# Performance work log

Measured on AMD Instinct MI355X. Metric: run time of the kernel, lower is better.

Reference implementation:

```python
import jax, jax.numpy as jnp
import numpy as np

N, E, D, H, C, B, G = 50000, 800000, 128, 256, 40, 3, 2
EPS = 1e-5


def setup_inputs() -> dict:
    key = jax.random.key(0)
    ks = jax.random.split(key, 32)
    rn = lambda k, s: jax.random.normal(k, s, dtype=jnp.float32)
    inp = {
        'x': rn(ks[0], (N, D)),
        'edge_index': jax.random.randint(ks[1], (2, E), 0, N, dtype=jnp.int64),
        'Wp': rn(ks[2], (D, H)), 'bp': rn(ks[3], (H,)),
        'W1l': rn(ks[4], (B, H, H)), 'b1l': rn(ks[5], (B, H)), 'W1r': rn(ks[6], (B, H, H)),
        'W2l': rn(ks[7], (B, H, H)), 'b2l': rn(ks[8], (B, H)), 'W2r': rn(ks[9], (B, H, H)),
        'bn1_g': rn(ks[10], (B, H)), 'bn1_b': rn(ks[11], (B, H)), 'bn1_m': rn(ks[12], (B, H)),
        'bn1_v': jax.random.uniform(ks[13], (B, H), dtype=jnp.float32),
        'bn2_g': rn(ks[14], (B, H)), 'bn2_b': rn(ks[15], (B, H)), 'bn2_m': rn(ks[16], (B, H)),
        'bn2_v': jax.random.uniform(ks[17], (B, H), dtype=jnp.float32),
        'gate_W': rn(ks[18], (G, H, H)), 'gate_b': rn(ks[19], (G, H)),
        'Wc1': rn(ks[20], (H, H // 2)), 'bc1': rn(ks[21], (H // 2,)),
        'Wc2': rn(ks[22], (H // 2, C)), 'bc2': rn(ks[23], (C,)),
    }
    return inp


def _sage(x, src, dst, Wl, bl, Wr):
    # PyG SAGEConv (mean aggr): lin_l(mean_{j in N(i)} x_j) + lin_r(x_i)
    agg = jax.ops.segment_sum(x[src], dst, num_segments=N)  # [N,H]
    cnt = jax.ops.segment_sum(jnp.ones((src.shape[0],), x.dtype), dst, num_segments=N)
    mean = agg / jnp.maximum(cnt, 1.0)[:, None]
    return mean @ Wl + bl + x @ Wr


def _bn(x, g, b, m, v):
    return (x - m) * (g * jax.lax.rsqrt(v + EPS)) + b


def reference(x, edge_index, Wp, bp, W1l, b1l, W1r, W2l, b2l, W2r,
              bn1_g, bn1_b, bn1_m, bn1_v, bn2_g, bn2_b, bn2_m, bn2_v,
              gate_W, gate_b, Wc1, bc1, Wc2, bc2):
    src, dst = edge_index[0], edge_index[1]
    prev = x @ Wp + bp  # input projection [N,H]
    for i in range(B):
        res = prev
        h = jax.nn.relu(_bn(_sage(prev, src, dst, W1l[i], b1l[i], W1r[i]),
                            bn1_g[i], bn1_b[i], bn1_m[i], bn1_v[i]))
        h = jax.nn.relu(_bn(_sage(h, src, dst, W2l[i], b2l[i], W2r[i]),
                            bn2_g[i], bn2_b[i], bn2_m[i], bn2_v[i]))
        cur = h + res
        if i > 0:
            gate = jax.nn.sigmoid(prev @ gate_W[i - 1] + gate_b[i - 1])
            cur = gate * prev + (1.0 - gate) * cur
        prev = cur
    return jax.nn.relu(prev @ Wc1 + bc1) @ Wc2 + bc2  # [N,C]
```

## Files before the change

kernel.cpp:

```cpp
#include <hip/hip_runtime.h>
#include <hip/hip_bf16.h>
#include <cstdint>

#define NNODES 50000
#define MPAD   50048
#define NEDGES 800000
#define DIN 128
#define HID 256
#define NCLS 40
#define NBLK 3
#define EPSV 1e-5f

typedef __bf16 bf16x8 __attribute__((ext_vector_type(8)));
typedef float  f32x4  __attribute__((ext_vector_type(4)));
typedef unsigned short us4v __attribute__((ext_vector_type(4)));
typedef unsigned short us8v __attribute__((ext_vector_type(8)));

__device__ __forceinline__ unsigned short bf_rtn(float x) {
  unsigned u = __float_as_uint(x);
  return (unsigned short)((u + 0x7fffu + ((u >> 16) & 1u)) >> 16);
}
__device__ __forceinline__ float bf_f(unsigned short h) {
  return __uint_as_float((unsigned)h << 16);
}
__device__ __forceinline__ void split4(float4 a, us4v& h, us4v& m, us4v& l) {
  float v[4] = {a.x, a.y, a.z, a.w};
#pragma unroll
  for (int i = 0; i < 4; i++) {
    unsigned short hh = bf_rtn(v[i]);
    float r1 = v[i] - bf_f(hh);
    unsigned short mm = bf_rtn(r1);
    float r2 = r1 - bf_f(mm);
    h[i] = hh; m[i] = mm; l[i] = bf_rtn(r2);
  }
}

__device__ __forceinline__ void glds16(const void* gsrc, void* ldst) {
  __builtin_amdgcn_global_load_lds((const __attribute__((address_space(1))) void*)gsrc,
                                   (__attribute__((address_space(3))) void*)ldst,
                                   16, 0, 0);
}

__global__ void hist_kernel(const int* __restrict__ dst, int* __restrict__ cnt, int E) {
  int e = blockIdx.x * blockDim.x + threadIdx.x;
  if (e < E) atomicAdd(&cnt[dst[e]], 1);
}

__global__ void scan_kernel(const int* __restrict__ cnt, int* __restrict__ row_ptr,
                            float* __restrict__ inv_cnt, int N) {
  __shared__ int sums[1024];
  int t = threadIdx.x;
  int chunk = (N + 1023) >> 10;
  int beg = t * chunk;
  int end = beg + chunk; if (end > N) end = N;
  int s = 0;
  for (int i = beg; i < end; ++i) s += cnt[i];
  sums[t] = s;
  __syncthreads();
  for (int off = 1; off < 1024; off <<= 1) {
    int v = 0;
    if (t >= off) v = sums[t - off];
    __syncthreads();
    sums[t] += v;
    __syncthreads();
  }
  int run = (t == 0) ? 0 : sums[t - 1];
  for (int i = beg; i < end; ++i) {
    row_ptr[i] = run;
    int c = cnt[i];
    inv_cnt[i] = 1.0f / (float)(c > 0 ? c : 1);
    run += c;
  }
  if (t == 1023) row_ptr[N] = run;
}

__global__ void fill_kernel(const int* __restrict__ src, const int* __restrict__ dst,
                            const int* __restrict__ row_ptr, int* __restrict__ fillc,
                            int* __restrict__ col, int E) {
  int e = blockIdx.x * blockDim.x + threadIdx.x;
  if (e < E) {
    int d = dst[e];
    int pos = atomicAdd(&fillc[d], 1);
    col[row_ptr[d] + pos] = src[e];
  }
}

__global__ __launch_bounds__(256)
void agg_kernel(const float* __restrict__ x, float* __restrict__ out,
                const int* __restrict__ row_ptr, const int* __restrict__ col,
                const float* __restrict__ inv_cnt) {
  int n = blockIdx.x;
  int h = threadIdx.x;
  int beg = row_ptr[n], end = row_ptr[n + 1];
  float s = 0.0f;
  for (int j = beg; j < end; ++j) {
    int c = col[j];
    s += x[(long)c * HID + h];
  }
  out[(long)n * HID + h] = s * inv_cnt[n];
}

__global__ void fold_kernel(const float* __restrict__ b1l, const float* __restrict__ g1,
                            const float* __restrict__ bb1, const float* __restrict__ m1,
                            const float* __restrict__ v1,
                            const float* __restrict__ b2l, const float* __restrict__ g2,
                            const float* __restrict__ bb2, const float* __restrict__ m2,
                            const float* __restrict__ v2,
                            float* __restrict__ S1, float* __restrict__ T1,
                            float* __restrict__ S2, float* __restrict__ T2) {
  int idx = blockIdx.x * 256 + threadIdx.x;
  float s1 = g1[idx] * rsqrtf(v1[idx] + EPSV);
  S1[idx] = s1;
  T1[idx] = (b1l[idx] - m1[idx]) * s1 + bb1[idx];
  float s2 = g2[idx] * rsqrtf(v2[idx] + EPSV);
  S2[idx] = s2;
  T2[idx] = (b2l[idx] - m2[idx]) * s2 + bb2[idx];
}

#define PREP_TOTAL 368640
struct PrepDescs {
  const float* src[16];
  unsigned dst_off[16];
  int N[16];
  int cum[16];
};
__global__ __launch_bounds__(256)
void prep_kernel(PrepDescs pd, char* out) {
  int i = blockIdx.x * 256 + threadIdx.x;
  if (i >= PREP_TOTAL) return;
  int j = 0;
  while (i >= pd.cum[j]) j++;
  int li = i - (j ? pd.cum[j - 1] : 0);
  int c = li % 12;
  int t = li / 12;
  int N = pd.N[j];
  int n = t % N;
  int kt = t / N;
  const float* src = pd.src[j];
  char* base = out + pd.dst_off[j] + (size_t)kt * N * 192;
  int p, k8;
  size_t addr;
  if (c < 8) {
    int d = c ^ (n & 7);
    p = d >> 2; k8 = d & 3;
    addr = (size_t)n * 128 + (size_t)c * 16;
  } else {
    p = 2; k8 = c - 8;
    addr = (size_t)N * 128 + ((size_t)k8 * N + n) * 16;
  }
  us8v v;
#pragma unroll
  for (int xj = 0; xj < 8; xj++) {
    float w = src[(size_t)(kt * 32 + k8 * 8 + xj) * N + n];
    unsigned short h = bf_rtn(w);
    if (p == 0) { v[xj] = h; continue; }
    float r1 = w - bf_f(h);
    unsigned short m = bf_rtn(r1);
    v[xj] = (p == 1) ? m : bf_rtn(r1 - bf_f(m));
  }
  *reinterpret_cast<us8v*>(base + addr) = v;
}

template<int BN, bool GATED>
__global__ __launch_bounds__(256)
void gemm_mfma(const float* __restrict__ A1, const char* __restrict__ B1, int K1,
               const float* __restrict__ A2, const char* __restrict__ B2, int K2,
               const char* __restrict__ BG, const float* __restrict__ Gb,
               const float* __restrict__ Sc, const float* __restrict__ Tc,
               const float* __restrict__ resid, float* __restrict__ C,
               int Mguard, int do_relu) {
  constexpr int NT = BN / 64;
  constexpr int NG = (BN * 48) / 1024;
  __shared__ __align__(16) unsigned short A_lds[64][104];
  __shared__ __align__(16) char B_lds[BN * 192];
  const int tid  = threadIdx.x;
  const int wv   = tid >> 6;
  const int lane = tid & 63;
  const int l15  = lane & 15;
  const int quad = lane >> 4;
  const int m0   = blockIdx.x * 64;
  const int sm  = tid >> 3;
  const int skc = (tid & 7) * 4;

  f32x4 acc1[4][NT];
#pragma unroll
  for (int i = 0; i < 4; i++)
#pragma unroll
    for (int j = 0; j < NT; j++) acc1[i][j] = (f32x4){0.f, 0.f, 0.f, 0.f};
  f32x4 acc2[GATED ? 4 : 1][GATED ? NT : 1];
  if constexpr (GATED) {
#pragma unroll
    for (int i = 0; i < 4; i++)
#pragma unroll
      for (int j = 0; j < NT; j++) acc2[i][j] = (f32x4){0.f, 0.f, 0.f, 0.f};
  }

  auto phase = [&](const float* __restrict__ A, const char* __restrict__ Bp,
                   int K, f32x4 (&acc)[4][NT]) {
    const int KT = K / 32;
    const bool g0 = (m0 + sm) < Mguard;
    const bool g1 = (m0 + 32 + sm) < Mguard;
    const float* ap0 = A + (size_t)(m0 + sm) * K + skc;
    const float* ap1 = A + (size_t)(m0 + 32 + sm) * K + skc;
    for (int kt = 0; kt < KT; ++kt) {
      __syncthreads();
      const char* bsrc = Bp + (size_t)kt * (BN * 192) + wv * (BN * 48) + (size_t)lane * 16;
      char* bdst = B_lds + wv * (BN * 48);
#pragma unroll
      for (int j = 0; j < NG; ++j)
        glds16(bsrc + j * 1024, bdst + j * 1024);
      float4 a0 = make_float4(0.f, 0.f, 0.f, 0.f), a1 = a0;
      if (g0) a0 = *reinterpret_cast<const float4*>(ap0 + kt * 32);
      if (g1) a1 = *reinterpret_cast<const float4*>(ap1 + kt * 32);
      us4v h4, m4, l4;
      split4(a0, h4, m4, l4);
      *reinterpret_cast<us4v*>(&A_lds[sm][skc])      = h4;
      *reinterpret_cast<us4v*>(&A_lds[sm][32 + skc]) = m4;
      *reinterpret_cast<us4v*>(&A_lds[sm][64 + skc]) = l4;
      split4(a1, h4, m4, l4);
      *reinterpret_cast<us4v*>(&A_lds[32 + sm][skc])      = h4;
      *reinterpret_cast<us4v*>(&A_lds[32 + sm][32 + skc]) = m4;
      *reinterpret_cast<us4v*>(&A_lds[32 + sm][64 + skc]) = l4;
      __syncthreads();
      bf16x8 ah[4], am[4], al[4];
#pragma unroll
      for (int mt = 0; mt < 4; mt++) {
        const unsigned short* rp = &A_lds[mt * 16 + l15][0];
        ah[mt] = *reinterpret_cast<const bf16x8*>(rp + quad * 8);
        am[mt] = *reinterpret_cast<const bf16x8*>(rp + 32 + quad * 8);
        al[mt] = *reinterpret_cast<const bf16x8*>(rp + 64 + quad * 8);
      }
#pragma unroll
      for (int nt = 0; nt < NT; nt++) {
        int n = wv * (BN / 4) + nt * 16 + l15;
        int sw = n & 7;
        const char* rb = B_lds + (size_t)n * 128;
        bf16x8 bh = *reinterpret_cast<const bf16x8*>(rb + ((quad ^ sw) * 16));
        bf16x8 bm = *reinterpret_cast<const bf16x8*>(rb + (((4 + quad) ^ sw) * 16));
        bf16x8 bl = *reinterpret_cast<const bf16x8*>(
            B_lds + (size_t)BN * 128 + ((size_t)quad * BN + n) * 16);
#pragma unroll
        for (int mt = 0; mt < 4; mt++) {
          acc[mt][nt] = __builtin_amdgcn_mfma_f32_16x16x32_bf16(ah[mt], bh, acc[mt][nt], 0, 0, 0);
          acc[mt][nt] = __builtin_amdgcn_mfma_f32_16x16x32_bf16(ah[mt], bm, acc[mt][nt], 0, 0, 0);
          acc[mt][nt] = __builtin_amdgcn_mfma_f32_16x16x32_bf16(am[mt], bh, acc[mt][nt], 0, 0, 0);
          acc[mt][nt] = __builtin_amdgcn_mfma_f32_16x16x32_bf16(am[mt], bm, acc[mt][nt], 0, 0, 0);
          acc[mt][nt] = __builtin_amdgcn_mfma_f32_16x16x32_bf16(ah[mt], bl, acc[mt][nt], 0, 0, 0);
          acc[mt][nt] = __builtin_amdgcn_mfma_f32_16x16x32_bf16(al[mt], bh, acc[mt][nt], 0, 0, 0);
        }
      }
    }
  };

  phase(A1, B1, K1, acc1);
  if (A2) phase(A2, B2, K2, acc1);
  if constexpr (GATED) phase(resid, BG, HID, acc2);

#pragma unroll
  for (int nt = 0; nt < NT; nt++) {
    int colc = wv * (BN / 4) + nt * 16 + l15;
    float sc = Sc ? Sc[colc] : 1.0f;
    float tc = Tc[colc];
    float gb = 0.0f;
    if constexpr (GATED) gb = Gb[colc];
#pragma unroll
    for (int mt = 0; mt < 4; mt++) {
#pragma unroll
      for (int r = 0; r < 4; r++) {
        int row = m0 + mt * 16 + quad * 4 + r;
        size_t base = (size_t)row * BN + colc;
        float v = acc1[mt][nt][r] * sc + tc;
        if (do_relu) v = fmaxf(v, 0.0f);
        if constexpr (GATED) {
          float p = resid[base];
          float g = 1.0f / (1.0f + __expf(-(acc2[mt][nt][r] + gb)));
          v = g * p + (1.0f - g) * (v + p);
        } else if (resid) {
          v += resid[base];
        }
        C[base] = v;
      }
    }
  }
}

__global__ __launch_bounds__(256)
void classifier2(const float* __restrict__ Tin, const float* __restrict__ W,
                 const float* __restrict__ bias, float* __restrict__ out, int M) {
  __shared__ float Ws[DIN * NCLS];
  __shared__ float bs[NCLS];
  __shared__ float Ts[64][DIN + 4];
  int tid = threadIdx.x;
  for (int i = tid; i < DIN * NCLS; i += 256) Ws[i] = W[i];
  if (tid < NCLS) bs[tid] = bias[tid];
  int row0 = blockIdx.x * 64;
  for (int idx = tid; idx < 64 * (DIN / 4); idx += 256) {
    int r = idx / (DIN / 4);
    int c4 = idx % (DIN / 4);
    float4 v = make_float4(0.f, 0.f, 0.f, 0.f);
    if (row0 + r < M) v = *reinterpret_cast<const float4*>(Tin + (long)(row0 + r) * DIN + c4 * 4);
    *reinterpret_cast<float4*>(&Ts[r][c4 * 4]) = v;
  }
  __syncthreads();
  int r = tid >> 2;
  int c0 = (tid & 3) * 10;
  float s[10];
#pragma unroll
  for (int c = 0; c < 10; c++) s[c] = bs[c0 + c];
  for (int k = 0; k < DIN; k++) {
    float a = Ts[r][k];
#pragma unroll
    for (int c = 0; c < 10; c++) s[c] = fmaf(a, Ws[k * NCLS + c0 + c], s[c]);
  }
  if (row0 + r < M) {
#pragma unroll
    for (int c = 0; c < 10; c++) out[(long)(row0 + r) * NCLS + c0 + c] = s[c];
  }
}

extern "C" void kernel_launch(void* const* d_in, const int* in_sizes, int n_in,
                              void* d_out, int out_size, void* d_ws, size_t ws_size,
                              hipStream_t stream) {
  const float* x      = (const float*)d_in[0];
  const int*   ei     = (const int*)d_in[1];
  const float* Wp     = (const float*)d_in[2];
  const float* bp     = (const float*)d_in[3];
  const float* W1l    = (const float*)d_in[4];
  const float* b1l    = (const float*)d_in[5];
  const float* W1r    = (const float*)d_in[6];
  const float* W2l    = (const float*)d_in[7];
  const float* b2l    = (const float*)d_in[8];
  const float* W2r    = (const float*)d_in[9];
  const float* bn1_g  = (const float*)d_in[10];
  const float* bn1_b  = (const float*)d_in[11];
  const float* bn1_m  = (const float*)d_in[12];
  const float* bn1_v  = (const float*)d_in[13];
  const float* bn2_g  = (const float*)d_in[14];
  const float* bn2_b  = (const float*)d_in[15];
  const float* bn2_m  = (const float*)d_in[16];
  const float* bn2_v  = (const float*)d_in[17];
  const float* gate_W = (const float*)d_in[18];
  const float* gate_b = (const float*)d_in[19];
  const float* Wc1    = (const float*)d_in[20];
  const float* bc1    = (const float*)d_in[21];
  const float* Wc2    = (const float*)d_in[22];
  const float* bc2    = (const float*)d_in[23];
  const int* srcp = ei;
  const int* dstp = ei + NEDGES;

  char* wsb = (char*)d_ws;
  size_t off = 0;
  auto alloc = [&](size_t bytes) -> void* {
    void* p = wsb + off;
    off += (bytes + 255) & ~(size_t)255;
    return p;
  };
  float* X0 = (float*)alloc((size_t)MPAD * HID * 4);
  float* X1 = (float*)alloc((size_t)MPAD * HID * 4);
  float* X2 = (float*)alloc((size_t)MPAD * HID * 4);
  char* prep = (char*)alloc(5898240);
  int* cnt     = (int*)alloc((size_t)NNODES * 4 * 2);
  int* fillc   = cnt + NNODES;
  int* row_ptr = (int*)alloc((size_t)(NNODES + 1) * 4);
  float* inv   = (float*)alloc((size_t)NNODES * 4);
  int* col     = (int*)alloc((size_t)NEDGES * 4);
  float* S1 = (float*)alloc(NBLK * HID * 4);
  float* T1 = (float*)alloc(NBLK * HID * 4);
  float* S2 = (float*)alloc(NBLK * HID * 4);
  float* T2 = (float*)alloc(NBLK * HID * 4);

  auto poff = [](int idx) -> unsigned {
    if (idx == 0) return 0;
    return 196608u + (unsigned)(idx - 1) * 393216u;
  };
  const char* prepWp  = prep + poff(0);
  auto prepW1l = [&](int i) { return prep + poff(1 + i); };
  auto prepW1r = [&](int i) { return prep + poff(4 + i); };
  auto prepW2l = [&](int i) { return prep + poff(7 + i); };
  auto prepW2r = [&](int i) { return prep + poff(10 + i); };
  auto prepGate = [&](int g) { return prep + poff(13 + g); };
  const char* prepWc1 = prep + poff(15);

  PrepDescs pd;
  {
    int c = 0, k = 0;
    auto add = [&](const float* s, int N, int chunks, unsigned doff) {
      pd.src[k] = s; pd.N[k] = N; c += chunks; pd.cum[k] = c; pd.dst_off[k] = doff; k++;
    };
    add(Wp, 256, 12288, poff(0));
    for (int i = 0; i < 3; i++) add(W1l + (size_t)i * 65536, 256, 24576, poff(1 + i));
    for (int i = 0; i < 3; i++) add(W1r + (size_t)i * 65536, 256, 24576, poff(4 + i));
    for (int i = 0; i < 3; i++) add(W2l + (size_t)i * 65536, 256, 24576, poff(7 + i));
    for (int i = 0; i < 3; i++) add(W2r + (size_t)i * 65536, 256, 24576, poff(10 + i));
    for (int g = 0; g < 2; g++) add(gate_W + (size_t)g * 65536, 256, 24576, poff(13 + g));
    add(Wc1, 128, 12288, poff(15));
  }

  hipMemsetAsync(cnt, 0, (size_t)NNODES * 4 * 2, stream);
  int eb = (NEDGES + 255) / 256;
  hist_kernel<<<eb, 256, 0, stream>>>(dstp, cnt, NEDGES);
  scan_kernel<<<1, 1024, 0, stream>>>(cnt, row_ptr, inv, NNODES);
  fill_kernel<<<eb, 256, 0, stream>>>(srcp, dstp, row_ptr, fillc, col, NEDGES);
  fold_kernel<<<3, 256, 0, stream>>>(b1l, bn1_g, bn1_b, bn1_m, bn1_v,
                                     b2l, bn2_g, bn2_b, bn2_m, bn2_v, S1, T1, S2, T2);
  prep_kernel<<<PREP_TOTAL / 256, 256, 0, stream>>>(pd, prep);

  int gm = MPAD / 64;
  gemm_mfma<256, false><<<gm, 256, 0, stream>>>(
      x, prepWp, DIN, nullptr, nullptr, 0, nullptr, nullptr,
      nullptr, bp, nullptr, X0, NNODES, 0);

  float* bufs[3] = {X0, X1, X2};
  int prev = 0;
  for (int i = 0; i < NBLK; ++i) {
    int bm = (prev + 1) % 3;
    int bh = (prev + 2) % 3;
    float* P  = bufs[prev];
    float* Mb = bufs[bm];
    float* Hb = bufs[bh];
    agg_kernel<<<NNODES, 256, 0, stream>>>(P, Mb, row_ptr, col, inv);
    gemm_mfma<256, false><<<gm, 256, 0, stream>>>(
        Mb, prepW1l(i), HID, P, prepW1r(i), HID, nullptr, nullptr,
        S1 + i * HID, T1 + i * HID, nullptr, Hb, MPAD, 1);
    agg_kernel<<<NNODES, 256, 0, stream>>>(Hb, Mb, row_ptr, col, inv);
    if (i == 0) {
      gemm_mfma<256, false><<<gm, 256, 0, stream>>>(
          Mb, prepW2l(0), HID, Hb, prepW2r(0), HID, nullptr, nullptr,
          S2, T2, P, Mb, MPAD, 1);
    } else {
      gemm_mfma<256, true><<<gm, 256, 0, stream>>>(
          Mb, prepW2l(i), HID, Hb, prepW2r(i), HID,
          prepGate(i - 1), gate_b + (size_t)(i - 1) * HID,
          S2 + i * HID, T2 + i * HID, P, Mb, MPAD, 1);
    }
    prev = bm;
  }
  float* P  = bufs[prev];
  float* Tb = bufs[(prev + 1) % 3];
  gemm_mfma<128, false><<<gm, 256, 0, stream>>>(
      P, prepWc1, HID, nullptr, nullptr, 0, nullptr, nullptr,
      nullptr, bc1, nullptr, Tb, MPAD, 1);
  classifier2<<<gm, 256, 0, stream>>>(Tb, Wc2, bc2, (float*)d_out, NNODES);
}
```

Before: 2.197 ms.

## Double-buffer GEMM LDS tiles and enlarge blocks to 512 threads with BM templating

Restructures the split-bf16 MFMA GEMM to double-buffer both A and B tiles in LDS. The next K-slice's global loads are issued before the current slice's MFMAs, so each k-step needs one barrier instead of two. Blocks grow to 8 waves with a configurable BM×BN tile (128 rows for most GEMMs, 64 for the gated one), raising per-block reuse of the B tiles. The cost is doubled LDS use per block and more registers per thread, which can lower occupancy. The grid for the mostly-memory-bound GEMMs also shrinks.

```diff
diff --git a/kernel.cpp b/kernel.cpp
--- a/kernel.cpp
+++ b/kernel.cpp
@@ -161,86 +161,117 @@
   *reinterpret_cast<us8v*>(base + addr) = v;
 }
 
-template<int BN, bool GATED>
-__global__ __launch_bounds__(256)
+template<int BM, int BN, bool GATED>
+__global__ __launch_bounds__(512)
 void gemm_mfma(const float* __restrict__ A1, const char* __restrict__ B1, int K1,
                const float* __restrict__ A2, const char* __restrict__ B2, int K2,
                const char* __restrict__ BG, const float* __restrict__ Gb,
                const float* __restrict__ Sc, const float* __restrict__ Tc,
                const float* __restrict__ resid, float* __restrict__ C,
                int Mguard, int do_relu) {
-  constexpr int NT = BN / 64;
-  constexpr int NG = (BN * 48) / 1024;
-  __shared__ __align__(16) unsigned short A_lds[64][104];
-  __shared__ __align__(16) char B_lds[BN * 192];
+  constexpr int WN = BN / 64;
+  constexpr int WM = 8 / WN;
+  constexpr int RB = BM / WM;
+  constexpr int MT = RB / 16;
+  constexpr int APITCH = 104;
+  constexpr int AL = (BM * 32) / 2048;
+  constexpr int NG = (BN * 24) / 1024;
+  __shared__ __align__(16) unsigned short A_lds[2][BM][APITCH];
+  __shared__ __align__(16) char B_lds[2][BN * 192];
   const int tid  = threadIdx.x;
   const int wv   = tid >> 6;
   const int lane = tid & 63;
   const int l15  = lane & 15;
   const int quad = lane >> 4;
-  const int m0   = blockIdx.x * 64;
-  const int sm  = tid >> 3;
-  const int skc = (tid & 7) * 4;
-
-  f32x4 acc1[4][NT];
-#pragma unroll
-  for (int i = 0; i < 4; i++)
-#pragma unroll
-    for (int j = 0; j < NT; j++) acc1[i][j] = (f32x4){0.f, 0.f, 0.f, 0.f};
-  f32x4 acc2[GATED ? 4 : 1][GATED ? NT : 1];
+  const int wm   = wv / WN;
+  const int wn   = wv % WN;
+  const int m0   = blockIdx.x * BM;
+  const int sr   = tid >> 3;
+  const int skc  = (tid & 7) * 4;
+
+  f32x4 acc1[MT][4];
+#pragma unroll
+  for (int i = 0; i < MT; i++)
+#pragma unroll
+    for (int j = 0; j < 4; j++) acc1[i][j] = (f32x4){0.f, 0.f, 0.f, 0.f};
+  f32x4 acc2[GATED ? MT : 1][GATED ? 4 : 1];
   if constexpr (GATED) {
 #pragma unroll
-    for (int i = 0; i < 4; i++)
-#pragma unroll
-      for (int j = 0; j < NT; j++) acc2[i][j] = (f32x4){0.f, 0.f, 0.f, 0.f};
-  }
+    for (int i = 0; i < MT; i++)
+#pragma unroll
+      for (int j = 0; j < 4; j++) acc2[i][j] = (f32x4){0.f, 0.f, 0.f, 0.f};
+  }
+
+  int buf = 0;
+
+  auto issueB = [&](const char* Bp, int kt, int b) {
+    const char* bsrc = Bp + (size_t)kt * (BN * 192) + wv * (BN * 24) + (size_t)lane * 16;
+    char* bdst = &B_lds[b][wv * (BN * 24)];
+#pragma unroll
+    for (int j = 0; j < NG; ++j)
+      glds16(bsrc + j * 1024, bdst + j * 1024);
+  };
+  auto storeA = [&](float4 (&a)[AL], int b) {
+#pragma unroll
+    for (int i = 0; i < AL; i++) {
+      us4v h4, m4, l4;
+      split4(a[i], h4, m4, l4);
+      unsigned short* rp = &A_lds[b][sr + i * 64][0];
+      *reinterpret_cast<us4v*>(rp + skc)      = h4;
+      *reinterpret_cast<us4v*>(rp + 32 + skc) = m4;
+      *reinterpret_cast<us4v*>(rp + 64 + skc) = l4;
+    }
+  };
 
   auto phase = [&](const float* __restrict__ A, const char* __restrict__ Bp,
-                   int K, f32x4 (&acc)[4][NT]) {
+                   int K, f32x4 (&acc)[MT][4]) {
     const int KT = K / 32;
-    const bool g0 = (m0 + sm) < Mguard;
-    const bool g1 = (m0 + 32 + sm) < Mguard;
-    const float* ap0 = A + (size_t)(m0 + sm) * K + skc;
-    const float* ap1 = A + (size_t)(m0 + 32 + sm) * K + skc;
+    bool g[AL];
+    const float* ap[AL];
+#pragma unroll
+    for (int i = 0; i < AL; i++) {
+      int row = m0 + sr + i * 64;
+      g[i] = row < Mguard;
+      ap[i] = A + (size_t)row * K + skc;
+    }
+    issueB(Bp, 0, buf);
+    {
+      float4 a[AL];
+#pragma unroll
+      for (int i = 0; i < AL; i++)
+        a[i] = g[i] ? *reinterpret_cast<const float4*>(ap[i]) : make_float4(0.f, 0.f, 0.f, 0.f);
+      storeA(a, buf);
+    }
     for (int kt = 0; kt < KT; ++kt) {
       __syncthreads();
-      const char* bsrc = Bp + (size_t)kt * (BN * 192) + wv * (BN * 48) + (size_t)lane * 16;
-      char* bdst = B_lds + wv * (BN * 48);
-#pragma unroll
-      for (int j = 0; j < NG; ++j)
-        glds16(bsrc + j * 1024, bdst + j * 1024);
-      float4 a0 = make_float4(0.f, 0.f, 0.f, 0.f), a1 = a0;
-      if (g0) a0 = *reinterpret_cast<const float4*>(ap0 + kt * 32);
-      if (g1) a1 = *reinterpret_cast<const float4*>(ap1 + kt * 32);
-      us4v h4, m4, l4;
-      split4(a0, h4, m4, l4);
-      *reinterpret_cast<us4v*>(&A_lds[sm][skc])      = h4;
-      *reinterpret_cast<us4v*>(&A_lds[sm][32 + skc]) = m4;
-      *reinterpret_cast<us4v*>(&A_lds[sm][64 + skc]) = l4;
-      split4(a1, h4, m4, l4);
-      *reinterpret_cast<us4v*>(&A_lds[32 + sm][skc])      = h4;
-      *reinterpret_cast<us4v*>(&A_lds[32 + sm][32 + skc]) = m4;
-      *reinterpret_cast<us4v*>(&A_lds[32 + sm][64 + skc]) = l4;
-      __syncthreads();
-      bf16x8 ah[4], am[4], al[4];
-#pragma unroll
-      for (int mt = 0; mt < 4; mt++) {
-        const unsigned short* rp = &A_lds[mt * 16 + l15][0];
+      const bool pf = (kt + 1 < KT);
+      float4 a[AL];
+      if (pf) {
+        issueB(Bp, kt + 1, buf ^ 1);
+#pragma unroll
+        for (int i = 0; i < AL; i++)
+          a[i] = g[i] ? *reinterpret_cast<const float4*>(ap[i] + (kt + 1) * 32)
+                      : make_float4(0.f, 0.f, 0.f, 0.f);
+      }
+      bf16x8 ah[MT], am[MT], al[MT];
+#pragma unroll
+      for (int mt = 0; mt < MT; mt++) {
+        const unsigned short* rp = &A_lds[buf][wm * RB + mt * 16 + l15][0];
         ah[mt] = *reinterpret_cast<const bf16x8*>(rp + quad * 8);
         am[mt] = *reinterpret_cast<const bf16x8*>(rp + 32 + quad * 8);
         al[mt] = *reinterpret_cast<const bf16x8*>(rp + 64 + quad * 8);
       }
 #pragma unroll
-      for (int nt = 0; nt < NT; nt++) {
-        int n = wv * (BN / 4) + nt * 16 + l15;
+      for (int nt = 0; nt < 4; nt++) {
+        int n = wn * 64 + nt * 16 + l15;
         int sw = n & 7;
-        const char* rb = B_lds + (size_t)n * 128;
+        const char* rb = &B_lds[buf][(size_t)n * 128];
         bf16x8 bh = *reinterpret_cast<const bf16x8*>(rb + ((quad ^ sw) * 16));
         bf16x8 bm = *reinterpret_cast<const bf16x8*>(rb + (((4 + quad) ^ sw) * 16));
         bf16x8 bl = *reinterpret_cast<const bf16x8*>(
-            B_lds + (size_t)BN * 128 + ((size_t)quad * BN + n) * 16);
-#pragma unroll
-        for (int mt = 0; mt < 4; mt++) {
+            &B_lds[buf][(size_t)BN * 128 + ((size_t)quad * BN + n) * 16]);
+#pragma unroll
+        for (int mt = 0; mt < MT; mt++) {
           acc[mt][nt] = __builtin_amdgcn_mfma_f32_16x16x32_bf16(ah[mt], bh, acc[mt][nt], 0, 0, 0);
           acc[mt][nt] = __builtin_amdgcn_mfma_f32_16x16x32_bf16(ah[mt], bm, acc[mt][nt], 0, 0, 0);
           acc[mt][nt] = __builtin_amdgcn_mfma_f32_16x16x32_bf16(am[mt], bh, acc[mt][nt], 0, 0, 0);
@@ -249,6 +280,8 @@
           acc[mt][nt] = __builtin_amdgcn_mfma_f32_16x16x32_bf16(al[mt], bh, acc[mt][nt], 0, 0, 0);
         }
       }
+      if (pf) storeA(a, buf ^ 1);
+      buf ^= 1;
     }
   };
 
@@ -257,17 +290,17 @@
   if constexpr (GATED) phase(resid, BG, HID, acc2);
 
 #pragma unroll
-  for (int nt = 0; nt < NT; nt++) {
-    int colc = wv * (BN / 4) + nt * 16 + l15;
+  for (int nt = 0; nt < 4; nt++) {
+    int colc = wn * 64 + nt * 16 + l15;
     float sc = Sc ? Sc[colc] : 1.0f;
     float tc = Tc[colc];
     float gb = 0.0f;
     if constexpr (GATED) gb = Gb[colc];
 #pragma unroll
-    for (int mt = 0; mt < 4; mt++) {
+    for (int mt = 0; mt < MT; mt++) {
 #pragma unroll
       for (int r = 0; r < 4; r++) {
-        int row = m0 + mt * 16 + quad * 4 + r;
+        int row = m0 + wm * RB + mt * 16 + quad * 4 + r;
         size_t base = (size_t)row * BN + colc;
         float v = acc1[mt][nt][r] * sc + tc;
         if (do_relu) v = fmaxf(v, 0.0f);
@@ -405,8 +438,9 @@
                                      b2l, bn2_g, bn2_b, bn2_m, bn2_v, S1, T1, S2, T2);
   prep_kernel<<<PREP_TOTAL / 256, 256, 0, stream>>>(pd, prep);
 
-  int gm = MPAD / 64;
-  gemm_mfma<256, false><<<gm, 256, 0, stream>>>(
+  int gm128 = MPAD / 128;
+  int gm64  = MPAD / 64;
+  gemm_mfma<128, 256, false><<<gm128, 512, 0, stream>>>(
       x, prepWp, DIN, nullptr, nullptr, 0, nullptr, nullptr,
       nullptr, bp, nullptr, X0, NNODES, 0);
 
@@ -419,16 +453,16 @@
     float* Mb = bufs[bm];
     float* Hb = bufs[bh];
     agg_kernel<<<NNODES, 256, 0, stream>>>(P, Mb, row_ptr, col, inv);
-    gemm_mfma<256, false><<<gm, 256, 0, stream>>>(
+    gemm_mfma<128, 256, false><<<gm128, 512, 0, stream>>>(
         Mb, prepW1l(i), HID, P, prepW1r(i), HID, nullptr, nullptr,
         S1 + i * HID, T1 + i * HID, nullptr, Hb, MPAD, 1);
     agg_kernel<<<NNODES, 256, 0, stream>>>(Hb, Mb, row_ptr, col, inv);
     if (i == 0) {
-      gemm_mfma<256, false><<<gm, 256, 0, stream>>>(
+      gemm_mfma<128, 256, false><<<gm128, 512, 0, stream>>>(
           Mb, prepW2l(0), HID, Hb, prepW2r(0), HID, nullptr, nullptr,
           S2, T2, P, Mb, MPAD, 1);
     } else {
-      gemm_mfma<256, true><<<gm, 256, 0, stream>>>(
+      gemm_mfma<64, 256, true><<<gm64, 512, 0, stream>>>(
           Mb, prepW2l(i), HID, Hb, prepW2r(i), HID,
           prepGate(i - 1), gate_b + (size_t)(i - 1) * HID,
           S2 + i * HID, T2 + i * HID, P, Mb, MPAD, 1);
@@ -437,8 +471,8 @@
   }
   float* P  = bufs[prev];
   float* Tb = bufs[(prev + 1) % 3];
-  gemm_mfma<128, false><<<gm, 256, 0, stream>>>(
+  gemm_mfma<128, 128, false><<<gm128, 512, 0, stream>>>(
       P, prepWc1, HID, nullptr, nullptr, 0, nullptr, nullptr,
       nullptr, bc1, nullptr, Tb, MPAD, 1);
-  classifier2<<<gm, 256, 0, stream>>>(Tb, Wc2, bc2, (float*)d_out, NNODES);
-}
+  classifier2<<<gm128 * 2, 256, 0, stream>>>(Tb, Wc2, bc2, (float*)d_out, NNODES);
+}
```

Result: faster. 2.124 ms (-3.3%).
